# Kernel tuning notes

Measured on AMD Instinct MI355X. Metric: run time of the kernel, lower is better.

The kernel has to match this reference:

```python
import jax, jax.numpy as jnp
import numpy as np

ROPE_BASE = 10000.0

def _rope_tables(T, head_dim, dtype):
    inv_freq = 1.0 / (ROPE_BASE ** (jnp.arange(0, head_dim, 2, dtype=jnp.float32) / head_dim))
    freqs = jnp.arange(T, dtype=jnp.float32)[:, None] * inv_freq[None, :]  # (T, hd/2)
    freqs = jnp.repeat(freqs, 2, axis=-1)  # (T, hd) interleaved (lucidrains-style)
    return jnp.cos(freqs).astype(dtype), jnp.sin(freqs).astype(dtype)

def _rotate_half(x):
    # interleaved pairs: (..., d) -> (-x2, x1) interleaved
    x = x.reshape(x.shape[:-1] + (-1, 2))
    x1, x2 = x[..., 0], x[..., 1]
    return jnp.stack((-x2, x1), axis=-1).reshape(x.shape[:-2] + (-1,))

def _apply_rope(x, cos, sin):
    # x: (B, H, T, hd); cos/sin: (T, hd)
    return x * cos[None, None] + _rotate_half(x) * sin[None, None]

def setup_inputs() -> dict:
    key = jax.random.key(0)
    k1, k2, k3 = jax.random.split(key, 3)
    B, T, C = 4, 2048, 1024
    x = jax.random.normal(k1, (B, T, C), dtype=jnp.float32)
    W_attn = jax.random.normal(k2, (C, 3 * C), dtype=jnp.float32) * 0.02
    W_proj = jax.random.normal(k3, (C, C), dtype=jnp.float32) * 0.02
    return {"x": x, "W_attn": W_attn, "W_proj": W_proj}

def reference(x, W_attn, W_proj):
    B, T, C = x.shape
    n_head = 16
    hd = C // n_head
    qkv = x @ W_attn  # (B, T, 3C)
    q, k, v = jnp.split(qkv, 3, axis=-1)
    # (B, T, H, hd) -> (B, H, T, hd)
    q = q.reshape(B, T, n_head, hd).transpose(0, 2, 1, 3)
    k = k.reshape(B, T, n_head, hd).transpose(0, 2, 1, 3)
    v = v.reshape(B, T, n_head, hd).transpose(0, 2, 1, 3)
    cos, sin = _rope_tables(T, hd, x.dtype)
    q = _apply_rope(q, cos, sin)
    k = _apply_rope(k, cos, sin)
    att = jnp.einsum('bhqd,bhkd->bhqk', q, k) * (1.0 / jnp.sqrt(jnp.array(hd, dtype=x.dtype)))
    causal = jnp.tril(jnp.ones((T, T), dtype=bool))
    att = jnp.where(causal[None, None], att, jnp.array(-jnp.inf, dtype=att.dtype))
    att = jax.nn.softmax(att, axis=-1)
    y = jnp.einsum('bhqk,bhkd->bhqd', att, v)
    y = y.transpose(0, 2, 1, 3).reshape(B, T, C)
    return y @ W_proj
```

## Files before the change

kernel.cpp:

```cpp
#include <hip/hip_runtime.h>
#include <hip/hip_bf16.h>
#include <math.h>

#define BB 4
#define TT 2048
#define CC 1024
#define NH 16
#define HD 64
#define C3 3072
#define LDK 72

#define QSCALE 0.18033688011112042f

typedef __attribute__((ext_vector_type(8))) short bf16x8;
typedef __attribute__((ext_vector_type(4))) short bf16x4;
typedef __attribute__((ext_vector_type(4))) float f32x4;

__device__ __forceinline__ void gload_lds16(const __hip_bfloat16* g, __hip_bfloat16* s) {
    __builtin_amdgcn_global_load_lds((const __attribute__((address_space(1))) void*)g,
                                     (__attribute__((address_space(3))) void*)s, 16, 0, 0);
}

__global__ __launch_bounds__(256) void rope_tables(float2* __restrict__ tab) {
    int idx = blockIdx.x * 256 + threadIdx.x;
    int t = idx >> 5;
    int p = idx & 31;
    float invf = exp2f((float)p * (-13.287712379549449f / 32.0f));
    float ang = (float)t * invf;
    float s, c;
    sincosf(ang, &s, &c);
    tab[idx] = make_float2(c, s);
}

__global__ __launch_bounds__(256) void cast_bf16x8(const float* __restrict__ X,
                                                   __hip_bfloat16* __restrict__ Y) {
    size_t i = ((size_t)blockIdx.x * 256 + threadIdx.x) * 8;
    float4 a = *(const float4*)(X + i);
    float4 b = *(const float4*)(X + i + 4);
    __align__(16) __hip_bfloat16 tmp[8];
    tmp[0] = __float2bfloat16(a.x);
    tmp[1] = __float2bfloat16(a.y);
    tmp[2] = __float2bfloat16(a.z);
    tmp[3] = __float2bfloat16(a.w);
    tmp[4] = __float2bfloat16(b.x);
    tmp[5] = __float2bfloat16(b.y);
    tmp[6] = __float2bfloat16(b.z);
    tmp[7] = __float2bfloat16(b.w);
    *(bf16x8*)(Y + i) = *(bf16x8*)tmp;
}

__global__ __launch_bounds__(256) void wtrans(const float* __restrict__ W,
                                              __hip_bfloat16* __restrict__ Wt,
                                              int K, int N) {
    __shared__ float st[64][65];
    const int n0 = blockIdx.x * 64;
    const int k0 = blockIdx.y * 64;
    const int tid = threadIdx.x;
    const int r = tid >> 4;
    const int c4 = (tid & 15) * 4;
#pragma unroll
    for (int p = 0; p < 4; ++p) {
        int k = p * 16 + r;
        float4 v = *(const float4*)(W + (size_t)(k0 + k) * N + n0 + c4);
        st[c4 + 0][k] = v.x;
        st[c4 + 1][k] = v.y;
        st[c4 + 2][k] = v.z;
        st[c4 + 3][k] = v.w;
    }
    __syncthreads();
    const int rr = tid >> 3;
    const int cc = (tid & 7) * 8;
#pragma unroll
    for (int p = 0; p < 2; ++p) {
        int n = p * 32 + rr;
        __align__(16) __hip_bfloat16 tmp[8];
#pragma unroll
        for (int j = 0; j < 8; ++j) tmp[j] = __float2bfloat16(st[n][cc + j]);
        *(bf16x8*)(Wt + (size_t)(n0 + n) * K + k0 + cc) = *(bf16x8*)tmp;
    }
}

#define CA0 0
#define CA1 1
#define CB0 2
#define CB1 3

#define BAR() __builtin_amdgcn_s_barrier()
#define SB0() __builtin_amdgcn_sched_barrier(0)
#define WAIT_LGKM0() do { asm volatile("s_waitcnt lgkmcnt(0)" ::: "memory"); SB0(); } while (0)
#define WAIT_VM4()   do { asm volatile("s_waitcnt vmcnt(4)" ::: "memory");  SB0(); } while (0)
#define WAIT_VM0()   do { asm volatile("s_waitcnt vmcnt(0)" ::: "memory");  SB0(); } while (0)

#define CLAMP_TS(x) ((x) < NTILE ? (x) : (x) - 2)

#define STAGE(gbase, h, ts, buf, cid) do {                                            \
    const __hip_bfloat16* _s = (gbase) + (size_t)((h) * 128 + w * 16) * K + (ts) * 64; \
    __hip_bfloat16* _d = &lds[buf][cid][w * 1024];                                    \
    gload_lds16(_s, _d);                                                              \
    gload_lds16(_s + 32, _d + 512);                                                   \
} while (0)

#define FRAGP(buf, cid, rowsub, ks)                                                   \
    ((const bf16x8*)((const char*)&lds[buf][cid][0] +                                 \
        (((rowsub) * 2 + (ks)) << 10) + (l16 << 6) + swzoff))

#define READ_A(buf, mi) do {                                                          \
    _Pragma("unroll") for (int _m = 0; _m < 4; ++_m)                                  \
    _Pragma("unroll") for (int _k = 0; _k < 2; ++_k)                                  \
        af[_m][_k] = *FRAGP(buf, wm, (mi) * 4 + _m, _k);                              \
} while (0)

#define READ_B(buf, ni) do {                                                          \
    _Pragma("unroll") for (int _n = 0; _n < 2; ++_n)                                  \
    _Pragma("unroll") for (int _k = 0; _k < 2; ++_k)                                  \
        bfr[(ni) * 2 + _n][_k] =                                                      \
            *FRAGP(buf, 2 + (wn >> 1), (wn & 1) * 4 + (ni) * 2 + _n, _k);             \
} while (0)

#define MFMA_Q(mb, nb) do {                                                           \
    __builtin_amdgcn_s_setprio(1);                                                    \
    _Pragma("unroll") for (int _m = 0; _m < 4; ++_m)                                  \
    _Pragma("unroll") for (int _n = 0; _n < 2; ++_n)                                  \
    _Pragma("unroll") for (int _k = 0; _k < 2; ++_k)                                  \
        acc[(mb) * 4 + _m][(nb) * 2 + _n] = __builtin_amdgcn_mfma_f32_16x16x32_bf16(  \
            af[_m][_k], bfr[(nb) * 2 + _n][_k], acc[(mb) * 4 + _m][(nb) * 2 + _n],    \
            0, 0, 0);                                                                 \
    __builtin_amdgcn_s_setprio(0);                                                    \
} while (0)

#define HALF_ITER(BUF, T12, B12, T34, B34) do {                                       \
                                                                 \
    READ_A(BUF, 0);                                                                   \
    READ_B(BUF, 0);                                                                   \
    STAGE(Bb, 1, CLAMP_TS(T12), B12, CB1);                                            \
    BAR(); WAIT_LGKM0();                                                              \
    MFMA_Q(0, 0);                                                                     \
    BAR();                                                                            \
                                                                 \
    READ_B(BUF, 1);                                                                   \
    STAGE(Ab, 1, CLAMP_TS(T12), B12, CA1);                                            \
    BAR(); WAIT_LGKM0();                                                              \
    MFMA_Q(0, 1);                                                                     \
    BAR();                                                                            \
                                                                 \
    READ_A(BUF, 1);                                                                   \
    STAGE(Bb, 0, CLAMP_TS(T34), B34, CB0);                                            \
    BAR(); WAIT_LGKM0();                                                              \
    MFMA_Q(1, 0);                                                                     \
    BAR();                                                                            \
                                                                 \
    STAGE(Ab, 0, CLAMP_TS(T34), B34, CA0);                                            \
    BAR(); WAIT_LGKM0();                                                              \
    MFMA_Q(1, 1);                                                                     \
    WAIT_VM4();                                                                       \
    BAR(); SB0();                                                                     \
} while (0)

#define GEMM256_BODY                                                                  \
    __shared__ __align__(16) __hip_bfloat16 lds[2][4][8192];             \
    const int tid = threadIdx.x;                                                      \
    const int w = tid >> 6;                                                           \
    const int lane = tid & 63;                                                        \
    const int l16 = lane & 15;                                                        \
    const int quad = lane >> 4;                                                       \
    const int wm = w >> 2;                                                            \
    const int wn = w & 3;                                                             \
    const int swzoff = ((quad * 8) ^ ((l16 & 8) << 1)) << 1;                          \
    const int bm0 = blockIdx.y * 256;                                                 \
    const int bn0 = blockIdx.x * 256;                                                 \
    const int NTILE = K >> 6;                                                         \
    const size_t laneOff = (size_t)(lane >> 2) * K +                                  \
                           (((lane & 3) * 8) ^ ((lane >> 5) << 4));                   \
    const __hip_bfloat16* Ab = A + (size_t)bm0 * K + laneOff;                         \
    const __hip_bfloat16* Bb = Bt + (size_t)bn0 * K + laneOff;                        \
    f32x4 acc[8][4] = {};                                                             \
             \
    STAGE(Bb, 0, 0, 0, CB0);                                                          \
    STAGE(Ab, 0, 0, 0, CA0);                                                          \
    STAGE(Bb, 1, 0, 0, CB1);                                                          \
    STAGE(Ab, 1, 0, 0, CA1);                                                          \
    STAGE(Bb, 0, 1, 1, CB0);                                                          \
    STAGE(Ab, 0, 1, 1, CA0);                                                          \
    WAIT_VM4();                                                                       \
    BAR(); SB0();                                                                     \
    for (int it = 0; it < NTILE / 2; ++it) {                                          \
        const int t = it * 2;                                                         \
        bf16x8 af[4][2], bfr[4][2];                                                   \
        HALF_ITER(0, t + 1, 1, t + 2, 0);                                             \
        HALF_ITER(1, t + 2, 0, t + 3, 1);                                             \
    }

__global__ __launch_bounds__(512) void gemm256_qkv_rope(const __hip_bfloat16* __restrict__ A,
                                                        const __hip_bfloat16* __restrict__ Bt,
                                                        const float2* __restrict__ tab,
                                                        __hip_bfloat16* __restrict__ C,
                                                        int M, int N, int K) {
    GEMM256_BODY

    if (bn0 < 2048) {
        const float qsc = (bn0 < 1024) ? QSCALE : 1.0f;
        const float sgn = (l16 & 1) ? 1.0f : -1.0f;
#pragma unroll
        for (int mt = 0; mt < 8; ++mt) {
            int row = bm0 + wm * 128 + mt * 16 + quad * 4;
#pragma unroll
            for (int nt = 0; nt < 4; ++nt) {
                int col = bn0 + wn * 64 + nt * 16 + l16;
                int p2 = nt * 8 + (l16 >> 1);
#pragma unroll
                for (int r = 0; r < 4; ++r) {
                    float own = acc[mt][nt][r];
                    float part = __shfl_xor(own, 1);
                    int trow = (row + r) & (TT - 1);
                    float2 cs = tab[(trow << 5) + p2];
                    float res = (own * cs.x + sgn * part * cs.y) * qsc;
                    C[(size_t)(row + r) * N + col] = __float2bfloat16(res);
                }
            }
        }
    } else {
#pragma unroll
        for (int mt = 0; mt < 8; ++mt) {
            int row = bm0 + wm * 128 + mt * 16 + quad * 4;
#pragma unroll
            for (int nt = 0; nt < 4; ++nt) {
                int col = bn0 + wn * 64 + nt * 16 + l16;
#pragma unroll
                for (int r = 0; r < 4; ++r)
                    C[(size_t)(row + r) * N + col] = __float2bfloat16(acc[mt][nt][r]);
            }
        }
    }
}

__global__ __launch_bounds__(512) void gemm256_f32(const __hip_bfloat16* __restrict__ A,
                                                   const __hip_bfloat16* __restrict__ Bt,
                                                   float* __restrict__ C,
                                                   int M, int N, int K) {
    GEMM256_BODY
#pragma unroll
    for (int mt = 0; mt < 8; ++mt) {
        int row = bm0 + wm * 128 + mt * 16 + quad * 4;
#pragma unroll
        for (int nt = 0; nt < 4; ++nt) {
            int col = bn0 + wn * 64 + nt * 16 + l16;
#pragma unroll
            for (int r = 0; r < 4; ++r)
                C[(size_t)(row + r) * N + col] = acc[mt][nt][r];
        }
    }
}

__global__ __launch_bounds__(256) void vtranspose(const __hip_bfloat16* __restrict__ qkvb,
                                                  __hip_bfloat16* __restrict__ vtb) {
    __shared__ __align__(16) __hip_bfloat16 st[64][LDK];
    const int bh = blockIdx.x >> 5;
    const int tt = blockIdx.x & 31;
    const int b = bh >> 4;
    const int h = bh & 15;
    const int tid = threadIdx.x;
    const int row = tid >> 3;
    const int a = tid & 7;
    const int col8 = a * 8;

#pragma unroll
    for (int pass = 0; pass < 2; ++pass) {
        int t = pass * 32 + row;
        *(bf16x8*)(&st[t][col8]) =
            *(const bf16x8*)(qkvb + ((size_t)(b * TT + tt * 64 + t)) * C3 + 2 * CC + h * HD + col8);
    }
    __syncthreads();
    const int h32 = (a >> 2) & 1;
    const int m4  = (a >> 1) & 1;
    const int p0 = h32 * 32 + ((2 * a) & 3) * 8 + m4 * 4;
    const int p1 = h32 * 32 + ((2 * a + 1) & 3) * 8 + m4 * 4;
#pragma unroll
    for (int pass = 0; pass < 2; ++pass) {
        int d = pass * 32 + row;
        __align__(16) __hip_bfloat16 tmp[8];
#pragma unroll
        for (int j = 0; j < 8; ++j) tmp[j] = st[col8 + j][d];
        __hip_bfloat16* dst = vtb + ((size_t)bh * HD + d) * TT + tt * 64;
        *(bf16x4*)(dst + p0) = *(const bf16x4*)&tmp[0];
        *(bf16x4*)(dst + p1) = *(const bf16x4*)&tmp[4];
    }
}

__global__ __launch_bounds__(256) void attn_mfma9(const __hip_bfloat16* __restrict__ qkvb,
                                                  const __hip_bfloat16* __restrict__ vtb,
                                                  __hip_bfloat16* __restrict__ y) {
    __shared__ __align__(16) __hip_bfloat16 Kb[3][64 * 64];
    __shared__ __align__(16) __hip_bfloat16 Vb[3][64 * 64];

    const int tid = threadIdx.x;
    const int w = tid >> 6;
    const int lane = tid & 63;
    const int l16 = lane & 15;
    const int quad = lane >> 4;
    const int swz = l16 & 7;

    const int rb = blockIdx.x;
    const int lb = (rb & 7) * 64 + (rb >> 3);
    const int bh = lb >> 3;
    const int pr = lb & 7;
    const int b = bh >> 4;
    const int h = bh & 15;

    const int sr = (lane >> 3) & 7;
    const int sc = lane & 7;
    const int klog = (sc ^ sr) * 8;

    const __hip_bfloat16* kbase = qkvb + (size_t)b * TT * C3 + CC + h * HD + klog;
    const __hip_bfloat16* vbase = vtb + (size_t)bh * HD * TT + klog;

#define ATTN_STAGE(t, bidx) do {                                                  \
    _Pragma("unroll")                                                             \
    for (int half = 0; half < 2; ++half) {                                        \
        int kr = w * 16 + half * 8 + sr;                                          \
        gload_lds16(kbase + (size_t)((t) * 64 + kr) * C3,                         \
                    Kb[bidx] + (w * 16 + half * 8) * 64);                         \
        gload_lds16(vbase + (size_t)kr * TT + (t) * 64,                           \
                    Vb[bidx] + (w * 16 + half * 8) * 64);                         \
    }                                                                             \
} while (0)

#pragma unroll
    for (int seg = 0; seg < 2; ++seg) {
        const int qblk = (seg == 0) ? (15 - pr) : pr;
        const int qb = qblk * 128;
        const int jtmax = 2 * qblk + 1;
        const int qn0 = qb + w * 32;
        const int qn1 = qn0 + 16;

        bf16x8 qf[2][2];
#pragma unroll
        for (int qt = 0; qt < 2; ++qt) {
            const __hip_bfloat16* qp = qkvb + (size_t)(b * TT + qn0 + qt * 16 + l16) * C3 + h * HD;
            qf[qt][0] = *(const bf16x8*)(qp + quad * 8);
            qf[qt][1] = *(const bf16x8*)(qp + 32 + quad * 8);
        }

        f32x4 O[2][4] = {};
        float l_q[2] = {0.f, 0.f};

        __syncthreads();
        ATTN_STAGE(0, 0);
        ATTN_STAGE(1, 1);

        int bcur = 0;
        for (int jt = 0; jt <= jtmax; ++jt) {
            if (jt < jtmax) { WAIT_VM4(); } else { WAIT_VM0(); }
            BAR(); SB0();

            if (jt + 2 <= jtmax) {
                const int bs = (bcur >= 1) ? (bcur - 1) : 2;
                ATTN_STAGE(jt + 2, bs);
            }

            const __hip_bfloat16* Kp = Kb[bcur];
            const __hip_bfloat16* Vp = Vb[bcur];

            const bool sk0 = (jt * 64 > qn0 + 15);
            const bool sk1 = (jt * 64 > qn1 + 15);

            if (!sk1) {
                f32x4 St[2][4] = {};
                __builtin_amdgcn_s_setprio(1);
#pragma unroll
                for (int ks = 0; ks < 2; ++ks) {
#pragma unroll
                    for (int mt = 0; mt < 4; ++mt) {
                        bf16x8 kf = *(const bf16x8*)(Kp + (mt * 16 + l16) * 64 +
                                                     ((ks * 4 + quad) ^ swz) * 8);
                        St[0][mt] = __builtin_amdgcn_mfma_f32_16x16x32_bf16(kf, qf[0][ks], St[0][mt], 0, 0, 0);
                        St[1][mt] = __builtin_amdgcn_mfma_f32_16x16x32_bf16(kf, qf[1][ks], St[1][mt], 0, 0, 0);
                    }
                }
                __builtin_amdgcn_s_setprio(0);

                bf16x8 vf[4][2];
#pragma unroll
                for (int dt = 0; dt < 4; ++dt) {
                    vf[dt][0] = *(const bf16x8*)(Vp + (dt * 16 + l16) * 64 + ((quad) ^ swz) * 8);
                    vf[dt][1] = *(const bf16x8*)(Vp + (dt * 16 + l16) * 64 + ((4 + quad) ^ swz) * 8);
                }

#pragma unroll
                for (int qt = 0; qt < 2; ++qt) {
                    const bool skq = qt == 0 ? sk0 : sk1;
                    if (skq) continue;
                    const int qn = qt == 0 ? qn0 : qn1;
                    if (jt * 64 + 63 > qn) {
#pragma unroll
                        for (int mt = 0; mt < 4; ++mt) {
#pragma unroll
                            for (int r = 0; r < 4; ++r) {
                                int key = jt * 64 + mt * 16 + quad * 4 + r;
                                if (key > qn + l16) St[qt][mt][r] = -__builtin_inff();
                            }
                        }
                    }
                    float sum = 0.f;
                    union { bf16x8 v; __hip_bfloat162 hh[4]; } pk0, pk1;
#pragma unroll
                    for (int mt = 0; mt < 4; ++mt) {
                        float e0 = exp2f(St[qt][mt][0]);
                        float e1 = exp2f(St[qt][mt][1]);
                        float e2 = exp2f(St[qt][mt][2]);
                        float e3 = exp2f(St[qt][mt][3]);
                        sum += (e0 + e1) + (e2 + e3);
                        __hip_bfloat162 lo = __float22bfloat162_rn(make_float2(e0, e1));
                        __hip_bfloat162 hi = __float22bfloat162_rn(make_float2(e2, e3));
                        if (mt < 2) { pk0.hh[mt * 2] = lo; pk0.hh[mt * 2 + 1] = hi; }
                        else        { pk1.hh[(mt - 2) * 2] = lo; pk1.hh[(mt - 2) * 2 + 1] = hi; }
                    }
                    l_q[qt] += sum;

                    __builtin_amdgcn_s_setprio(1);
#pragma unroll
                    for (int dt = 0; dt < 4; ++dt) {
                        O[qt][dt] = __builtin_amdgcn_mfma_f32_16x16x32_bf16(pk0.v, vf[dt][0], O[qt][dt], 0, 0, 0);
                        O[qt][dt] = __builtin_amdgcn_mfma_f32_16x16x32_bf16(pk1.v, vf[dt][1], O[qt][dt], 0, 0, 0);
                    }
                    __builtin_amdgcn_s_setprio(0);
                }
            }

            bcur = (bcur == 2) ? 0 : bcur + 1;
        }

#pragma unroll
        for (int qt = 0; qt < 2; ++qt) {
            float l2 = l_q[qt];
            l2 += __shfl_xor(l2, 16);
            l2 += __shfl_xor(l2, 32);
            float lO[4];
#pragma unroll
            for (int r = 0; r < 4; ++r) lO[r] = 1.0f / __shfl(l2, quad * 4 + r);
            const int qbase = qn0 + qt * 16 + quad * 4;
#pragma unroll
            for (int dt = 0; dt < 4; ++dt) {
#pragma unroll
                for (int r = 0; r < 4; ++r) {
                    y[(size_t)(b * TT + qbase + r) * CC + h * HD + dt * 16 + l16] =
                        __float2bfloat16(O[qt][dt][r] * lO[r]);
                }
            }
        }
    }
#undef ATTN_STAGE
}

extern "C" void kernel_launch(void* const* d_in, const int* in_sizes, int n_in,
                              void* d_out, int out_size, void* d_ws, size_t ws_size,
                              hipStream_t stream) {
    const float* x      = (const float*)d_in[0];
    const float* W_attn = (const float*)d_in[1];
    const float* W_proj = (const float*)d_in[2];
    float* out = (float*)d_out;

    const size_t NBT = (size_t)BB * TT;
    __hip_bfloat16* xb   = (__hip_bfloat16*)d_ws;
    __hip_bfloat16* qkvb = xb + NBT * CC;
    __hip_bfloat16* vtb  = qkvb + NBT * C3;
    __hip_bfloat16* Wab  = vtb + NBT * CC;
    __hip_bfloat16* Wpb  = Wab + (size_t)CC * C3;
    float2* tab          = (float2*)(Wpb + (size_t)CC * CC);
    __hip_bfloat16* yb   = xb;

    const int M = BB * TT;

    rope_tables<<<dim3(TT * 32 / 256), 256, 0, stream>>>(tab);
    cast_bf16x8<<<dim3((int)(NBT * CC / 2048)), 256, 0, stream>>>(x, xb);
    wtrans<<<dim3(C3 / 64, CC / 64), 256, 0, stream>>>(W_attn, Wab, CC, C3);
    wtrans<<<dim3(CC / 64, CC / 64), 256, 0, stream>>>(W_proj, Wpb, CC, CC);

    gemm256_qkv_rope<<<dim3(C3 / 256, M / 256), 512, 0, stream>>>(xb, Wab, tab, qkvb, M, C3, CC);

    vtranspose<<<dim3(BB * NH * (TT / 64)), 256, 0, stream>>>(qkvb, vtb);

    attn_mfma9<<<dim3(BB * NH * 8), 256, 0, stream>>>(qkvb, vtb, yb);

    gemm256_f32<<<dim3(CC / 256, M / 256), 512, 0, stream>>>(yb, Wpb, out, M, CC, CC);
}
```

Measured before the change: 281.8 us.

## Remap QKV GEMM blocks for XCD locality and use 128x256 tiles for projection

The QKV GEMM launch becomes a 1D grid whose block index is remapped so that consecutive blocks on each of the 8 XCDs cover neighbouring output tiles, aiming to improve L2 reuse of the A and B panels. The output projection GEMM moves from 256x256 tiles (128 blocks, fewer than the CU count) to a new 128x256-tile kernel with 256 blocks, with the same XCD-aware remap. It has its own LDS staging layout and pipeline waits. The aim is to fill more CUs on the small projection GEMM, at the cost of less data reuse per block and a new hand-written staging schedule.

```diff
diff --git a/kernel.cpp b/kernel.cpp
--- a/kernel.cpp
+++ b/kernel.cpp
@@ -89,6 +89,7 @@
 #define SB0() __builtin_amdgcn_sched_barrier(0)
 #define WAIT_LGKM0() do { asm volatile("s_waitcnt lgkmcnt(0)" ::: "memory"); SB0(); } while (0)
 #define WAIT_VM4()   do { asm volatile("s_waitcnt vmcnt(4)" ::: "memory");  SB0(); } while (0)
+#define WAIT_VM3()   do { asm volatile("s_waitcnt vmcnt(3)" ::: "memory");  SB0(); } while (0)
 #define WAIT_VM0()   do { asm volatile("s_waitcnt vmcnt(0)" ::: "memory");  SB0(); } while (0)
 
 #define CLAMP_TS(x) ((x) < NTILE ? (x) : (x) - 2)
@@ -166,8 +167,6 @@
     const int wm = w >> 2;                                                            \
     const int wn = w & 3;                                                             \
     const int swzoff = ((quad * 8) ^ ((l16 & 8) << 1)) << 1;                          \
-    const int bm0 = blockIdx.y * 256;                                                 \
-    const int bn0 = blockIdx.x * 256;                                                 \
     const int NTILE = K >> 6;                                                         \
     const size_t laneOff = (size_t)(lane >> 2) * K +                                  \
                            (((lane & 3) * 8) ^ ((lane >> 5) << 4));                   \
@@ -195,6 +194,10 @@
                                                         const float2* __restrict__ tab,
                                                         __hip_bfloat16* __restrict__ C,
                                                         int M, int N, int K) {
+    const int lin = blockIdx.x;
+    const int nl = (lin & 7) * 48 + (lin >> 3);
+    const int bn0 = (nl % 12) * 256;
+    const int bm0 = (nl / 12) * 256;
     GEMM256_BODY
 
     if (bn0 < 2048) {
@@ -233,14 +236,116 @@
     }
 }
 
-__global__ __launch_bounds__(512) void gemm256_f32(const __hip_bfloat16* __restrict__ A,
+__global__ __launch_bounds__(512) void gemm128_f32(const __hip_bfloat16* __restrict__ A,
                                                    const __hip_bfloat16* __restrict__ Bt,
                                                    float* __restrict__ C,
                                                    int M, int N, int K) {
-    GEMM256_BODY
-#pragma unroll
-    for (int mt = 0; mt < 8; ++mt) {
-        int row = bm0 + wm * 128 + mt * 16 + quad * 4;
+    __shared__ __align__(16) __hip_bfloat16 lds[2][24576];
+    const int tid = threadIdx.x;
+    const int w = tid >> 6;
+    const int lane = tid & 63;
+    const int l16 = lane & 15;
+    const int quad = lane >> 4;
+    const int wm = w >> 2;
+    const int wn = w & 3;
+    const int swzoff = ((quad * 8) ^ ((l16 & 8) << 1)) << 1;
+    const int lin = blockIdx.x;
+    const int nl = (lin & 7) * 32 + (lin >> 3);
+    const int bn0 = (nl & 3) * 256;
+    const int bm0 = (nl >> 2) * 128;
+    const int NTILE = K >> 6;
+    const int aswz = ((lane & 3) * 8) ^ ((lane >> 5) << 4);
+    const size_t laneOff = (size_t)(lane >> 2) * K + aswz;
+    const __hip_bfloat16* Ab = A + (size_t)bm0 * K;
+    const __hip_bfloat16* Bb = Bt + (size_t)bn0 * K + laneOff;
+    f32x4 acc[4][4] = {};
+
+#define STAGE_A128(h, ts, buf) do {                                                   \
+    const __hip_bfloat16* _s = Ab + (size_t)((h) * 64 + (w & 3) * 16 + (lane >> 2)) * K \
+                               + (ts) * 64 + (w >> 2) * 32 + aswz;                    \
+    gload_lds16(_s, &lds[buf][(h) * 4096 + ((w & 3) * 2 + (w >> 2)) * 512]);          \
+} while (0)
+
+#define STAGE_B128(h, ts, buf) do {                                                   \
+    const __hip_bfloat16* _s = Bb + (size_t)((h) * 128 + w * 16) * K + (ts) * 64;     \
+    __hip_bfloat16* _d = &lds[buf][8192 + (h) * 8192 + w * 1024];                     \
+    gload_lds16(_s, _d);                                                              \
+    gload_lds16(_s + 32, _d + 512);                                                   \
+} while (0)
+
+#define FRAGA128(buf, m_, ks)                                                         \
+    ((const bf16x8*)((const char*)&lds[buf][wm * 4096] +                              \
+        ((((m_) * 2 + (ks)) << 10) + (l16 << 6) + swzoff)))
+#define FRAGB128(buf, n_, ks)                                                         \
+    ((const bf16x8*)((const char*)&lds[buf][8192 + (wn >> 1) * 8192] +                \
+        (((((wn & 1) * 4 + (n_)) * 2 + (ks)) << 10) + (l16 << 6) + swzoff)))
+
+#define READA128(buf, mi) do {                                                        \
+    _Pragma("unroll") for (int _m = 0; _m < 2; ++_m)                                  \
+    _Pragma("unroll") for (int _k = 0; _k < 2; ++_k)                                  \
+        af[(mi) * 2 + _m][_k] = *FRAGA128(buf, (mi) * 2 + _m, _k);                    \
+} while (0)
+
+#define READB128(buf, ni) do {                                                        \
+    _Pragma("unroll") for (int _n = 0; _n < 2; ++_n)                                  \
+    _Pragma("unroll") for (int _k = 0; _k < 2; ++_k)                                  \
+        bfr[(ni) * 2 + _n][_k] = *FRAGB128(buf, (ni) * 2 + _n, _k);                   \
+} while (0)
+
+#define MFMA8(mb, nb) do {                                                            \
+    __builtin_amdgcn_s_setprio(1);                                                    \
+    _Pragma("unroll") for (int _m = 0; _m < 2; ++_m)                                  \
+    _Pragma("unroll") for (int _n = 0; _n < 2; ++_n)                                  \
+    _Pragma("unroll") for (int _k = 0; _k < 2; ++_k)                                  \
+        acc[(mb) * 2 + _m][(nb) * 2 + _n] = __builtin_amdgcn_mfma_f32_16x16x32_bf16(  \
+            af[(mb) * 2 + _m][_k], bfr[(nb) * 2 + _n][_k],                            \
+            acc[(mb) * 2 + _m][(nb) * 2 + _n], 0, 0, 0);                              \
+    __builtin_amdgcn_s_setprio(0);                                                    \
+} while (0)
+
+#define HALF128(BUF, T12, B12, T34, B34) do {                                         \
+    READA128(BUF, 0);                                                                 \
+    READB128(BUF, 0);                                                                 \
+    STAGE_B128(1, CLAMP_TS(T12), B12);                                                \
+    BAR(); WAIT_LGKM0();                                                              \
+    MFMA8(0, 0);                                                                      \
+    BAR();                                                                            \
+    READB128(BUF, 1);                                                                 \
+    STAGE_A128(1, CLAMP_TS(T12), B12);                                                \
+    BAR(); WAIT_LGKM0();                                                              \
+    MFMA8(0, 1);                                                                      \
+    BAR();                                                                            \
+    READA128(BUF, 1);                                                                 \
+    STAGE_B128(0, CLAMP_TS(T34), B34);                                                \
+    BAR(); WAIT_LGKM0();                                                              \
+    MFMA8(1, 0);                                                                      \
+    BAR();                                                                            \
+    STAGE_A128(0, CLAMP_TS(T34), B34);                                                \
+    BAR(); WAIT_LGKM0();                                                              \
+    MFMA8(1, 1);                                                                      \
+    WAIT_VM3();                                                                       \
+    BAR(); SB0();                                                                     \
+} while (0)
+
+    STAGE_B128(0, 0, 0);
+    STAGE_A128(0, 0, 0);
+    STAGE_B128(1, 0, 0);
+    STAGE_A128(1, 0, 0);
+    STAGE_B128(0, 1, 1);
+    STAGE_A128(0, 1, 1);
+    WAIT_VM3();
+    BAR(); SB0();
+    for (int it = 0; it < NTILE / 2; ++it) {
+        const int t = it * 2;
+        bf16x8 af[4][2], bfr[4][2];
+        HALF128(0, t + 1, 1, t + 2, 0);
+        HALF128(1, t + 2, 0, t + 3, 1);
+    }
+    WAIT_VM0();
+
+#pragma unroll
+    for (int mt = 0; mt < 4; ++mt) {
+        int row = bm0 + wm * 64 + mt * 16 + quad * 4;
 #pragma unroll
         for (int nt = 0; nt < 4; ++nt) {
             int col = bn0 + wn * 64 + nt * 16 + l16;
@@ -249,6 +354,14 @@
                 C[(size_t)(row + r) * N + col] = acc[mt][nt][r];
         }
     }
+#undef STAGE_A128
+#undef STAGE_B128
+#undef FRAGA128
+#undef FRAGB128
+#undef READA128
+#undef READB128
+#undef MFMA8
+#undef HALF128
 }
 
 __global__ __launch_bounds__(256) void vtranspose(const __hip_bfloat16* __restrict__ qkvb,
@@ -475,11 +588,11 @@
     wtrans<<<dim3(C3 / 64, CC / 64), 256, 0, stream>>>(W_attn, Wab, CC, C3);
     wtrans<<<dim3(CC / 64, CC / 64), 256, 0, stream>>>(W_proj, Wpb, CC, CC);
 
-    gemm256_qkv_rope<<<dim3(C3 / 256, M / 256), 512, 0, stream>>>(xb, Wab, tab, qkvb, M, C3, CC);
+    gemm256_qkv_rope<<<dim3(384), 512, 0, stream>>>(xb, Wab, tab, qkvb, M, C3, CC);
 
     vtranspose<<<dim3(BB * NH * (TT / 64)), 256, 0, stream>>>(qkvb, vtb);
 
     attn_mfma9<<<dim3(BB * NH * 8), 256, 0, stream>>>(qkvb, vtb, yb);
 
-    gemm256_f32<<<dim3(CC / 256, M / 256), 512, 0, stream>>>(yb, Wpb, out, M, CC, CC);
-}
+    gemm128_f32<<<dim3(256), 512, 0, stream>>>(yb, Wpb, out, M, CC, CC);
+}
```

Measured after the change: 271.9 us. 3.5% less time.
